# Performance work log

Measured on AMD Instinct MI355X. Metric: run time of the kernel, lower is better.

Reference implementation:

```python
import jax, jax.numpy as jnp
import numpy as np

N = 50000      # nodes
E = 800000     # edges (avg degree 16)
D = 64         # dim_inner
L = 2          # layers_mp
OUT = 2        # dim_out (fraud / not fraud)
LN_EPS = 1e-5


def setup_inputs() -> dict:
    key = jax.random.key(0)
    ks = jax.random.split(key, 12)
    rn = lambda k, shape: jax.random.normal(k, shape, dtype=jnp.float32) * 0.05
    return {
        "x": jax.random.normal(ks[0], (N, D), dtype=jnp.float32),
        "edge_attr": jax.random.normal(ks[1], (E, D), dtype=jnp.float32),
        "edge_index": jax.random.randint(ks[2], (2, E), 0, N),
        # GINEConv inner MLP: Linear(D,D) -> ReLU -> Linear(D,D), stacked over L layers
        "gine_w1": rn(ks[3], (L, D, D)), "gine_b1": jnp.zeros((L, D), jnp.float32),
        "gine_w2": rn(ks[4], (L, D, D)), "gine_b2": jnp.zeros((L, D), jnp.float32),
        # edge-update MLP: Linear(3D,D) -> ReLU -> Linear(D,D)
        "em_w1": rn(ks[5], (L, 3 * D, D)), "em_b1": jnp.zeros((L, D), jnp.float32),
        "em_w2": rn(ks[6], (L, D, D)), "em_b2": jnp.zeros((L, D), jnp.float32),
        # per-layer LayerNorm params
        "ln_g": jnp.ones((L, D), jnp.float32), "ln_b": jnp.zeros((L, D), jnp.float32),
        # post_mp head: Linear(D, OUT)
        "head_w": rn(ks[7], (D, OUT)), "head_b": jnp.zeros((OUT,), jnp.float32),
    }


def _layernorm(h, g, b):
    mu = h.mean(axis=-1, keepdims=True)
    var = h.var(axis=-1, keepdims=True)
    return (h - mu) * jax.lax.rsqrt(var + LN_EPS) * g + b


def reference(x, edge_attr, edge_index, gine_w1, gine_b1, gine_w2, gine_b2,
              em_w1, em_b1, em_w2, em_b2, ln_g, ln_b, head_w, head_b):
    src, dst = edge_index[0], edge_index[1]
    e = edge_attr
    for i in range(L):
        # GINEConv: sum_{j->i} relu(x_j + e_ji), eps=0 so (1+eps)*x_i = x_i
        msg = jax.nn.relu(x[src] + e)                         # [E, D] gather + fuse
        agg = jax.ops.segment_sum(msg, dst, num_segments=N)   # [N, D] scatter-add
        h = x + agg
        h = jax.nn.relu(h @ gine_w1[i] + gine_b1[i]) @ gine_w2[i] + gine_b2[i]
        # norm -> activation (dropout p=0 in eval)
        x = jax.nn.relu(_layernorm(h, ln_g[i], ln_b[i]))
        # edge update: e = e + emlp(cat[x_src, x_dst, e]) / 2
        cat = jnp.concatenate([x[src], x[dst], e], axis=-1)   # [E, 3D]
        e = e + (jax.nn.relu(cat @ em_w1[i] + em_b1[i]) @ em_w2[i] + em_b2[i]) * 0.5
    # post_mp head on node features
    return x @ head_w + head_b
```

## Files before the change

### kernel.cpp

```cpp
#include <hip/hip_runtime.h>
#include <hip/hip_bf16.h>

#define NN 50000
#define NE 800000
#define D 64
#define K3 (3 * D)
#define LNEPS 1e-5f
#define STR 68
#define SINB 200
#define SHB 72
#define SEB 68

typedef __attribute__((ext_vector_type(8))) short bf16x8;
typedef __attribute__((ext_vector_type(4))) float f32x4;

__device__ __forceinline__ unsigned cvt2(float lo, float hi) {
  __hip_bfloat162 h = __float22bfloat162_rn(make_float2(lo, hi));
  return *(unsigned*)&h;
}
__device__ __forceinline__ unsigned short f2bf(float f) {
  __hip_bfloat16 h = __float2bfloat16(f);
  return *(unsigned short*)&h;
}
__device__ __forceinline__ float bf2f(unsigned short s) {
  return __uint_as_float((unsigned)s << 16);
}

#define FMA4x4(v, w)                                                  \
  a0.x = fmaf(v.x, w.x, a0.x); a0.y = fmaf(v.x, w.y, a0.y);           \
  a0.z = fmaf(v.x, w.z, a0.z); a0.w = fmaf(v.x, w.w, a0.w);           \
  a1.x = fmaf(v.y, w.x, a1.x); a1.y = fmaf(v.y, w.y, a1.y);           \
  a1.z = fmaf(v.y, w.z, a1.z); a1.w = fmaf(v.y, w.w, a1.w);           \
  a2.x = fmaf(v.z, w.x, a2.x); a2.y = fmaf(v.z, w.y, a2.y);           \
  a2.z = fmaf(v.z, w.z, a2.z); a2.w = fmaf(v.z, w.w, a2.w);           \
  a3.x = fmaf(v.w, w.x, a3.x); a3.y = fmaf(v.w, w.y, a3.y);           \
  a3.z = fmaf(v.w, w.z, a3.z); a3.w = fmaf(v.w, w.w, a3.w);

#define FMA2x4(v, w)                                                  \
  a0.x = fmaf(v.x, w.x, a0.x); a0.y = fmaf(v.x, w.y, a0.y);           \
  a0.z = fmaf(v.x, w.z, a0.z); a0.w = fmaf(v.x, w.w, a0.w);           \
  a1.x = fmaf(v.y, w.x, a1.x); a1.y = fmaf(v.y, w.y, a1.y);           \
  a1.z = fmaf(v.y, w.z, a1.z); a1.w = fmaf(v.y, w.w, a1.w);

#define HSTORE_RELU(buf)                                              \
  buf[(j0+0)*STR + t0+0] = fmaxf(a0.x, 0.f);                          \
  buf[(j0+1)*STR + t0+0] = fmaxf(a0.y, 0.f);                          \
  buf[(j0+2)*STR + t0+0] = fmaxf(a0.z, 0.f);                          \
  buf[(j0+3)*STR + t0+0] = fmaxf(a0.w, 0.f);                          \
  buf[(j0+0)*STR + t0+1] = fmaxf(a1.x, 0.f);                          \
  buf[(j0+1)*STR + t0+1] = fmaxf(a1.y, 0.f);                          \
  buf[(j0+2)*STR + t0+1] = fmaxf(a1.z, 0.f);                          \
  buf[(j0+3)*STR + t0+1] = fmaxf(a1.w, 0.f);                          \
  buf[(j0+0)*STR + t0+2] = fmaxf(a2.x, 0.f);                          \
  buf[(j0+1)*STR + t0+2] = fmaxf(a2.y, 0.f);                          \
  buf[(j0+2)*STR + t0+2] = fmaxf(a2.z, 0.f);                          \
  buf[(j0+3)*STR + t0+2] = fmaxf(a2.w, 0.f);                          \
  buf[(j0+0)*STR + t0+3] = fmaxf(a3.x, 0.f);                          \
  buf[(j0+1)*STR + t0+3] = fmaxf(a3.y, 0.f);                          \
  buf[(j0+2)*STR + t0+3] = fmaxf(a3.z, 0.f);                          \
  buf[(j0+3)*STR + t0+3] = fmaxf(a3.w, 0.f);

__global__ __launch_bounds__(256) void count_kernel(
    const int* __restrict__ dst, int* __restrict__ deg) {
  int e = blockIdx.x * 256 + threadIdx.x;
  if (e < NE) atomicAdd(&deg[dst[e]], 1);
}

__global__ __launch_bounds__(1024) void scan_reduce_kernel(
    const int* __restrict__ deg, int* __restrict__ bsum) {
  __shared__ int sS[16];
  int i = blockIdx.x * 1024 + threadIdx.x;
  int v = (i < NN) ? deg[i] : 0;
#pragma unroll
  for (int o = 32; o > 0; o >>= 1) v += __shfl_down(v, o, 64);
  if ((threadIdx.x & 63) == 0) sS[threadIdx.x >> 6] = v;
  __syncthreads();
  if (threadIdx.x == 0) {
    int s = 0;
#pragma unroll
    for (int k = 0; k < 16; ++k) s += sS[k];
    bsum[blockIdx.x] = s;
  }
}

__global__ __launch_bounds__(1024) void scan_final_kernel(
    const int* __restrict__ deg, const int* __restrict__ bsum,
    int* __restrict__ off, int* __restrict__ cur) {
  __shared__ int sD[1024];
  __shared__ int sOfs;
  const int t = threadIdx.x;
  const int b = blockIdx.x;
  int i = b * 1024 + t;
  int v = (i < NN) ? deg[i] : 0;
  sD[t] = v;
  if (t == 0) {
    int o = 0;
    for (int k = 0; k < b; ++k) o += bsum[k];
    sOfs = o;
  }
  __syncthreads();
  for (int st = 1; st < 1024; st <<= 1) {
    int add = (t >= st) ? sD[t - st] : 0;
    __syncthreads();
    sD[t] += add;
    __syncthreads();
  }
  if (i < NN) {
    int excl = sOfs + sD[t] - v;
    off[i] = excl;
    cur[i] = excl;
    if (i == NN - 1) off[NN] = NE;
  }
}

__global__ __launch_bounds__(256) void fill_kernel(
    const int* __restrict__ src, const int* __restrict__ dst,
    int* __restrict__ cur, int2* __restrict__ epair,
    int* __restrict__ dcsr, int* __restrict__ pos) {
  int e = blockIdx.x * 256 + threadIdx.x;
  if (e < NE) {
    int d = dst[e];
    int p = atomicAdd(&cur[d], 1);
    epair[p] = make_int2(e, src[e]);
    dcsr[p] = d;
    pos[e] = p;
  }
}

__global__ __launch_bounds__(256) void permute_e_kernel(
    const float* __restrict__ e, const int* __restrict__ pos,
    unsigned short* __restrict__ ecsr) {
  int tid = blockIdx.x * 256 + threadIdx.x;
  int eid = tid >> 2, q = tid & 3;
  if (eid >= NE) return;
  int p = pos[eid];
  const float4* srcp = (const float4*)(e + (size_t)eid * D + q * 16);
  float4 v0 = srcp[0], v1 = srcp[1], v2 = srcp[2], v3 = srcp[3];
  uint4 u0, u1;
  u0.x = cvt2(v0.x, v0.y); u0.y = cvt2(v0.z, v0.w);
  u0.z = cvt2(v1.x, v1.y); u0.w = cvt2(v1.z, v1.w);
  u1.x = cvt2(v2.x, v2.y); u1.y = cvt2(v2.z, v2.w);
  u1.z = cvt2(v3.x, v3.y); u1.w = cvt2(v3.z, v3.w);
  uint4* dstp = (uint4*)(ecsr + (size_t)p * D + q * 16);
  dstp[0] = u0;
  dstp[1] = u1;
}

__global__ __launch_bounds__(256) void pack_weights_kernel(
    const float* __restrict__ w1, const float* __restrict__ w2,
    unsigned short* __restrict__ wB1, unsigned short* __restrict__ wB2) {
  int tid = blockIdx.x * 256 + threadIdx.x;
  const float* wsrc;
  unsigned short* wdst;
  int kb, j, slot;
  if (tid < 1536) {
    int nt = tid / 384, kk = (tid / 64) % 6, l = tid & 63;
    kb = kk * 32 + (l >> 4) * 8;
    j = nt * 16 + (l & 15);
    wsrc = w1; wdst = wB1; slot = tid;
  } else {
    int t = tid - 1536;
    int nt = t / 128, kk = (t / 64) & 1, l = t & 63;
    kb = kk * 32 + (l >> 4) * 8;
    j = nt * 16 + (l & 15);
    wsrc = w2; wdst = wB2; slot = t;
  }
  unsigned short b[8];
#pragma unroll
  for (int i = 0; i < 8; ++i) b[i] = f2bf(wsrc[(kb + i) * D + j]);
  uint4 v;
  v.x = (unsigned)b[0] | ((unsigned)b[1] << 16);
  v.y = (unsigned)b[2] | ((unsigned)b[3] << 16);
  v.z = (unsigned)b[4] | ((unsigned)b[5] << 16);
  v.w = (unsigned)b[6] | ((unsigned)b[7] << 16);
  *(uint4*)(wdst + (size_t)slot * 8) = v;
}

__device__ __forceinline__ void mlp_tail512(
    float* sIN, float* sH, float* sPS, float* sPQ, float* sMu, float* sRs,
    const float* __restrict__ w1, const float* __restrict__ b1,
    const float* __restrict__ w2, const float* __restrict__ b2,
    const float* __restrict__ g, const float* __restrict__ bln,
    float* __restrict__ xo, unsigned short* __restrict__ xob,
    const float* __restrict__ hw, const float* __restrict__ hb,
    float* __restrict__ outh,
    int n0, int tid) {
  __syncthreads();
  const int tj = tid & 15, tt = tid >> 4;
  const int j0 = tj * 4, t0 = tt * 2;
  float4 a0, a1;

  {
    float4 bv = *(const float4*)(b1 + j0);
    a0 = a1 = bv;
    for (int k = 0; k < D; ++k) {
      float4 w = *(const float4*)(w1 + k * D + j0);
      float2 v = *(const float2*)&sIN[k * STR + t0];
      FMA2x4(v, w)
    }
  }
  sH[(j0 + 0) * STR + t0 + 0] = fmaxf(a0.x, 0.f);
  sH[(j0 + 1) * STR + t0 + 0] = fmaxf(a0.y, 0.f);
  sH[(j0 + 2) * STR + t0 + 0] = fmaxf(a0.z, 0.f);
  sH[(j0 + 3) * STR + t0 + 0] = fmaxf(a0.w, 0.f);
  sH[(j0 + 0) * STR + t0 + 1] = fmaxf(a1.x, 0.f);
  sH[(j0 + 1) * STR + t0 + 1] = fmaxf(a1.y, 0.f);
  sH[(j0 + 2) * STR + t0 + 1] = fmaxf(a1.z, 0.f);
  sH[(j0 + 3) * STR + t0 + 1] = fmaxf(a1.w, 0.f);
  __syncthreads();

  {
    float4 bv = *(const float4*)(b2 + j0);
    a0 = a1 = bv;
    for (int k = 0; k < D; ++k) {
      float4 w = *(const float4*)(w2 + k * D + j0);
      float2 v = *(const float2*)&sH[k * STR + t0];
      FMA2x4(v, w)
    }
  }
  __syncthreads();
  *(float4*)&sH[(t0 + 0) * STR + j0] = a0;
  *(float4*)&sH[(t0 + 1) * STR + j0] = a1;
  __syncthreads();

  {
    const int t = tid & 63, p = tid >> 6;
    const float* r = &sH[t * STR + p * 8];
    float s = 0.f, q = 0.f;
#pragma unroll
    for (int i = 0; i < 8; ++i) { float v = r[i]; s += v; q = fmaf(v, v, q); }
    sPS[p * 64 + t] = s;
    sPQ[p * 64 + t] = q;
  }
  __syncthreads();
  if (tid < 64) {
    float s = 0.f, q = 0.f;
#pragma unroll
    for (int p = 0; p < 8; ++p) { s += sPS[p * 64 + tid]; q += sPQ[p * 64 + tid]; }
    float mu = s * (1.f / 64.f);
    float var = q * (1.f / 64.f) - mu * mu;
    sMu[tid] = mu;
    sRs[tid] = rsqrtf(var + LNEPS);
  }
  __syncthreads();

  {
    const int t = tid >> 3, c = (tid & 7) * 8;
    int node = n0 + t;
    if (node < NN) {
      float mu = sMu[t], rs = sRs[t];
      float4 v0 = *(const float4*)&sH[t * STR + c + 0];
      float4 v1 = *(const float4*)&sH[t * STR + c + 4];
      float4 g0v = *(const float4*)(g + c + 0);
      float4 g1v = *(const float4*)(g + c + 4);
      float4 b0v = *(const float4*)(bln + c + 0);
      float4 b1v = *(const float4*)(bln + c + 4);
      float4 r0, r1;
      r0.x = fmaxf(fmaf((v0.x - mu) * rs, g0v.x, b0v.x), 0.f);
      r0.y = fmaxf(fmaf((v0.y - mu) * rs, g0v.y, b0v.y), 0.f);
      r0.z = fmaxf(fmaf((v0.z - mu) * rs, g0v.z, b0v.z), 0.f);
      r0.w = fmaxf(fmaf((v0.w - mu) * rs, g0v.w, b0v.w), 0.f);
      r1.x = fmaxf(fmaf((v1.x - mu) * rs, g1v.x, b1v.x), 0.f);
      r1.y = fmaxf(fmaf((v1.y - mu) * rs, g1v.y, b1v.y), 0.f);
      r1.z = fmaxf(fmaf((v1.z - mu) * rs, g1v.z, b1v.z), 0.f);
      r1.w = fmaxf(fmaf((v1.w - mu) * rs, g1v.w, b1v.w), 0.f);
      if (outh) {
        float h0, h1;
        h0 = r0.x * hw[(c + 0) * 2 + 0] + r0.y * hw[(c + 1) * 2 + 0] +
             r0.z * hw[(c + 2) * 2 + 0] + r0.w * hw[(c + 3) * 2 + 0] +
             r1.x * hw[(c + 4) * 2 + 0] + r1.y * hw[(c + 5) * 2 + 0] +
             r1.z * hw[(c + 6) * 2 + 0] + r1.w * hw[(c + 7) * 2 + 0];
        h1 = r0.x * hw[(c + 0) * 2 + 1] + r0.y * hw[(c + 1) * 2 + 1] +
             r0.z * hw[(c + 2) * 2 + 1] + r0.w * hw[(c + 3) * 2 + 1] +
             r1.x * hw[(c + 4) * 2 + 1] + r1.y * hw[(c + 5) * 2 + 1] +
             r1.z * hw[(c + 6) * 2 + 1] + r1.w * hw[(c + 7) * 2 + 1];
#pragma unroll
        for (int o = 1; o < 8; o <<= 1) {
          h0 += __shfl_xor(h0, o, 64);
          h1 += __shfl_xor(h1, o, 64);
        }
        if ((tid & 7) == 0) {
          outh[node * 2 + 0] = h0 + hb[0];
          outh[node * 2 + 1] = h1 + hb[1];
        }
      } else {
        float* o = xo + (size_t)node * D + c;
        ((float4*)o)[0] = r0;
        ((float4*)o)[1] = r1;
        if (xob) {
          uint4 u;
          u.x = cvt2(r0.x, r0.y); u.y = cvt2(r0.z, r0.w);
          u.z = cvt2(r1.x, r1.y); u.w = cvt2(r1.z, r1.w);
          *(uint4*)(xob + (size_t)node * D + c) = u;
        }
      }
    }
  }
}

__global__ __launch_bounds__(512) void node_mlp_g0_kernel(
    const float* __restrict__ x, const unsigned short* __restrict__ ecsr,
    const int2* __restrict__ epair, const int* __restrict__ off,
    const float* __restrict__ w1, const float* __restrict__ b1,
    const float* __restrict__ w2, const float* __restrict__ b2,
    const float* __restrict__ g, const float* __restrict__ bln,
    float* __restrict__ xo, unsigned short* __restrict__ xob) {
  __shared__ float sIN[D * STR];
  __shared__ float sH[D * STR];
  __shared__ float sPS[512], sPQ[512], sMu[64], sRs[64];
  const int tid = threadIdx.x;
  const int n0 = blockIdx.x * 64;
  const int wv = tid >> 6, lane = tid & 63;
  for (int q = 0; q < 8; ++q) {
    int t = wv * 8 + q;
    int node = n0 + t;
    float acc = 0.f;
    if (node < NN) {
      acc = x[(size_t)node * D + lane];
      int beg = off[node], end = off[node + 1];
      const unsigned short* er = ecsr + (size_t)beg * D + lane;
      int cnt = end - beg, i = 0;
      for (; i + 3 < cnt; i += 4) {
        int s0 = epair[beg + i + 0].y, s1 = epair[beg + i + 1].y;
        int s2 = epair[beg + i + 2].y, s3 = epair[beg + i + 3].y;
        float xa = x[(size_t)s0 * D + lane], ea = bf2f(er[(size_t)(i + 0) * D]);
        float xb = x[(size_t)s1 * D + lane], eb = bf2f(er[(size_t)(i + 1) * D]);
        float xc = x[(size_t)s2 * D + lane], ec = bf2f(er[(size_t)(i + 2) * D]);
        float xd = x[(size_t)s3 * D + lane], ed = bf2f(er[(size_t)(i + 3) * D]);
        acc += (fmaxf(xa + ea, 0.f) + fmaxf(xb + eb, 0.f)) +
               (fmaxf(xc + ec, 0.f) + fmaxf(xd + ed, 0.f));
      }
      for (; i < cnt; ++i) {
        int s0 = epair[beg + i].y;
        acc += fmaxf(x[(size_t)s0 * D + lane] + bf2f(er[(size_t)i * D]), 0.f);
      }
    }
    sIN[lane * STR + t] = acc;
  }
  mlp_tail512(sIN, sH, sPS, sPQ, sMu, sRs, w1, b1, w2, b2, g, bln,
              xo, xob, nullptr, nullptr, nullptr, n0, tid);
}

__global__ __launch_bounds__(512) void node_mlp_g1_kernel(
    const float* __restrict__ x, const unsigned short* __restrict__ msg,
    const int* __restrict__ off,
    const float* __restrict__ w1, const float* __restrict__ b1,
    const float* __restrict__ w2, const float* __restrict__ b2,
    const float* __restrict__ g, const float* __restrict__ bln,
    const float* __restrict__ hw, const float* __restrict__ hb,
    float* __restrict__ outh) {
  __shared__ float sIN[D * STR];
  __shared__ float sH[D * STR];
  __shared__ float sPS[512], sPQ[512], sMu[64], sRs[64];
  const int tid = threadIdx.x;
  const int n0 = blockIdx.x * 64;
  const int wv = tid >> 6, lane = tid & 63;
  for (int q = 0; q < 8; ++q) {
    int t = wv * 8 + q;
    int node = n0 + t;
    float acc = 0.f;
    if (node < NN) {
      acc = x[(size_t)node * D + lane];
      int beg = off[node], end = off[node + 1];
      const unsigned short* mr = msg + (size_t)beg * D + lane;
      int cnt = end - beg, i = 0;
      for (; i + 3 < cnt; i += 4) {
        float m0 = bf2f(mr[(size_t)(i + 0) * D]);
        float m1 = bf2f(mr[(size_t)(i + 1) * D]);
        float m2 = bf2f(mr[(size_t)(i + 2) * D]);
        float m3 = bf2f(mr[(size_t)(i + 3) * D]);
        acc += (m0 + m1) + (m2 + m3);
      }
      for (; i < cnt; ++i) acc += bf2f(mr[(size_t)i * D]);
    }
    sIN[lane * STR + t] = acc;
  }
  mlp_tail512(sIN, sH, sPS, sPQ, sMu, sRs, w1, b1, w2, b2, g, bln,
              nullptr, nullptr, hw, hb, outh, n0, tid);
}

__global__ __launch_bounds__(256) void edge_mfma_csr_kernel(
    const unsigned short* __restrict__ x1b, const unsigned short* __restrict__ ecsr,
    const int2* __restrict__ epair, const int* __restrict__ dcsr,
    const unsigned short* __restrict__ wB1, const float* __restrict__ b1,
    const unsigned short* __restrict__ wB2, const float* __restrict__ b2,
    unsigned short* __restrict__ msg) {
  __shared__ unsigned short sIN[64 * SINB];
  __shared__ unsigned short sH[64 * SHB];

  const int tid = threadIdx.x;
  const int e0 = blockIdx.x * 64;
  const int lane = tid & 63;
  const int mt = tid >> 6;
  const int hl = lane >> 4;
  const int ll = lane & 15;

  {
    const int t = tid & 63, p = tid >> 6;
    int slot = e0 + t;
    int sN = epair[slot].y;
    int dN = dcsr[slot];
    const uint4* xs = (const uint4*)(x1b + (size_t)sN * D + p * 16);
    const uint4* xd = (const uint4*)(x1b + (size_t)dN * D + p * 16);
    const uint4* ec = (const uint4*)(ecsr + (size_t)slot * D + p * 16);
    uint4* r0 = (uint4*)(sIN + t * SINB + p * 16);
    uint4* r1 = (uint4*)(sIN + t * SINB + 64 + p * 16);
    uint4* r2 = (uint4*)(sIN + t * SINB + 128 + p * 16);
    uint4 a0v = xs[0], a1v = xs[1];
    uint4 b0v = xd[0], b1v = xd[1];
    uint4 c0v = ec[0], c1v = ec[1];
    r0[0] = a0v; r0[1] = a1v;
    r1[0] = b0v; r1[1] = b1v;
    r2[0] = c0v; r2[1] = c1v;
  }
  __syncthreads();

  f32x4 acc[4];
#pragma unroll
  for (int nt = 0; nt < 4; ++nt) {
    float b = b1[nt * 16 + ll];
    acc[nt].x = b; acc[nt].y = b; acc[nt].z = b; acc[nt].w = b;
  }
  {
    const unsigned short* aBase = sIN + (mt * 16 + ll) * SINB + hl * 8;
#pragma unroll
    for (int kk = 0; kk < 6; ++kk) {
      bf16x8 af = *(const bf16x8*)(aBase + kk * 32);
#pragma unroll
      for (int nt = 0; nt < 4; ++nt) {
        bf16x8 bf = *(const bf16x8*)(wB1 + ((size_t)(nt * 6 + kk) * 64 + lane) * 8);
        acc[nt] = __builtin_amdgcn_mfma_f32_16x16x32_bf16(af, bf, acc[nt], 0, 0, 0);
      }
    }
  }
#pragma unroll
  for (int nt = 0; nt < 4; ++nt)
#pragma unroll
    for (int r = 0; r < 4; ++r)
      sH[(mt * 16 + hl * 4 + r) * SHB + nt * 16 + ll] = f2bf(fmaxf(acc[nt][r], 0.f));
  __syncthreads();

  f32x4 acc2[4];
#pragma unroll
  for (int nt = 0; nt < 4; ++nt) {
    float b = b2[nt * 16 + ll];
    acc2[nt].x = b; acc2[nt].y = b; acc2[nt].z = b; acc2[nt].w = b;
  }
  {
    const unsigned short* hBase = sH + (mt * 16 + ll) * SHB + hl * 8;
#pragma unroll
    for (int kk = 0; kk < 2; ++kk) {
      bf16x8 af = *(const bf16x8*)(hBase + kk * 32);
#pragma unroll
      for (int nt = 0; nt < 4; ++nt) {
        bf16x8 bf = *(const bf16x8*)(wB2 + ((size_t)(nt * 2 + kk) * 64 + lane) * 8);
        acc2[nt] = __builtin_amdgcn_mfma_f32_16x16x32_bf16(af, bf, acc2[nt], 0, 0, 0);
      }
    }
  }

#pragma unroll
  for (int r = 0; r < 4; ++r) {
    int t = mt * 16 + hl * 4 + r;
    int slot = e0 + t;
    const unsigned short* xr = sIN + t * SINB;
    const unsigned short* er = sIN + t * SINB + 128;
    unsigned short* mr = msg + (size_t)slot * D;
#pragma unroll
    for (int nt = 0; nt < 4; ++nt) {
      int j = nt * 16 + ll;
      float xf = bf2f(xr[j]);
      float ef = bf2f(er[j]);
      mr[j] = f2bf(fmaxf(xf + fmaf(0.5f, acc2[nt][r], ef), 0.f));
    }
  }
}

__global__ __launch_bounds__(256) void scatter_kernel(
    const float* __restrict__ x, const float* __restrict__ e,
    const int* __restrict__ src, const int* __restrict__ dst,
    float* __restrict__ agg) {
  int tid = blockIdx.x * blockDim.x + threadIdx.x;
  if (tid >= NE * 16) return;
  int eid = tid >> 4, q = tid & 15;
  int s = src[eid], d = dst[eid];
  float4 xv = ((const float4*)(x + (size_t)s * D))[q];
  float4 ev = ((const float4*)(e + (size_t)eid * D))[q];
  float* a = agg + (size_t)d * D + q * 4;
  atomicAdd(a + 0, fmaxf(xv.x + ev.x, 0.f));
  atomicAdd(a + 1, fmaxf(xv.y + ev.y, 0.f));
  atomicAdd(a + 2, fmaxf(xv.z + ev.z, 0.f));
  atomicAdd(a + 3, fmaxf(xv.w + ev.w, 0.f));
}

__device__ __forceinline__ void mlp_tail256(
    float* sIN, float* sH, float* sPS, float* sPQ, float* sMu, float* sRs,
    const float* __restrict__ w1, const float* __restrict__ b1,
    const float* __restrict__ w2, const float* __restrict__ b2,
    const float* __restrict__ g, const float* __restrict__ bln,
    float* __restrict__ xo, int n0, int tid) {
  __syncthreads();
  const int tj = tid & 15, tt = tid >> 4;
  const int j0 = tj * 4, t0 = tt * 4;
  float4 a0, a1, a2, a3;
  {
    float4 bv = *(const float4*)(b1 + j0);
    a0 = a1 = a2 = a3 = bv;
    for (int k = 0; k < D; ++k) {
      float4 w = *(const float4*)(w1 + k * D + j0);
      float4 v = *(const float4*)&sIN[k * STR + t0];
      FMA4x4(v, w)
    }
  }
  HSTORE_RELU(sH)
  __syncthreads();
  {
    float4 bv = *(const float4*)(b2 + j0);
    a0 = a1 = a2 = a3 = bv;
    for (int k = 0; k < D; ++k) {
      float4 w = *(const float4*)(w2 + k * D + j0);
      float4 v = *(const float4*)&sH[k * STR + t0];
      FMA4x4(v, w)
    }
  }
  __syncthreads();
  *(float4*)&sH[(t0 + 0) * STR + j0] = a0;
  *(float4*)&sH[(t0 + 1) * STR + j0] = a1;
  *(float4*)&sH[(t0 + 2) * STR + j0] = a2;
  *(float4*)&sH[(t0 + 3) * STR + j0] = a3;
  __syncthreads();
  {
    const int t = tid & 63, p = tid >> 6;
    const float* r = &sH[t * STR + p * 16];
    float s = 0.f, q = 0.f;
#pragma unroll
    for (int i = 0; i < 16; ++i) { float v = r[i]; s += v; q = fmaf(v, v, q); }
    sPS[p * 64 + t] = s;
    sPQ[p * 64 + t] = q;
  }
  __syncthreads();
  if (tid < 64) {
    float s = sPS[tid] + sPS[64 + tid] + sPS[128 + tid] + sPS[192 + tid];
    float q = sPQ[tid] + sPQ[64 + tid] + sPQ[128 + tid] + sPQ[192 + tid];
    float mu = s * (1.f / 64.f);
    float var = q * (1.f / 64.f) - mu * mu;
    sMu[tid] = mu;
    sRs[tid] = rsqrtf(var + LNEPS);
  }
  __syncthreads();
  {
    const int t = tid >> 2, c = (tid & 3) * 16;
    int node = n0 + t;
    if (node < NN) {
      float mu = sMu[t], rs = sRs[t];
      float* o = xo + (size_t)node * D + c;
#pragma unroll
      for (int i = 0; i < 4; ++i) {
        float4 v = *(const float4*)&sH[t * STR + c + i * 4];
        float4 gv = *(const float4*)(g + c + i * 4);
        float4 bv = *(const float4*)(bln + c + i * 4);
        float4 r;
        r.x = fmaxf(fmaf((v.x - mu) * rs, gv.x, bv.x), 0.f);
        r.y = fmaxf(fmaf((v.y - mu) * rs, gv.y, bv.y), 0.f);
        r.z = fmaxf(fmaf((v.z - mu) * rs, gv.z, bv.z), 0.f);
        r.w = fmaxf(fmaf((v.w - mu) * rs, gv.w, bv.w), 0.f);
        ((float4*)o)[i] = r;
      }
    }
  }
}

__global__ __launch_bounds__(256) void node_mlp_kernel(
    const float* __restrict__ x, const float* __restrict__ agg,
    const float* __restrict__ w1, const float* __restrict__ b1,
    const float* __restrict__ w2, const float* __restrict__ b2,
    const float* __restrict__ g, const float* __restrict__ bln,
    float* __restrict__ xo) {
  __shared__ float sIN[D * STR];
  __shared__ float sH[D * STR];
  __shared__ float sPS[256], sPQ[256], sMu[64], sRs[64];
  const int tid = threadIdx.x;
  const int n0 = blockIdx.x * 64;
  {
    const int t = tid & 63, p = tid >> 6;
    int node = n0 + t;
    int cn = node < NN ? node : 0;
    const float* xr = x + (size_t)cn * D + p * 16;
    const float* ar = agg + (size_t)cn * D + p * 16;
#pragma unroll
    for (int i = 0; i < 4; ++i) {
      float4 xv = ((const float4*)xr)[i];
      float4 av = ((const float4*)ar)[i];
      int k = p * 16 + i * 4;
      sIN[(k + 0) * STR + t] = xv.x + av.x;
      sIN[(k + 1) * STR + t] = xv.y + av.y;
      sIN[(k + 2) * STR + t] = xv.z + av.z;
      sIN[(k + 3) * STR + t] = xv.w + av.w;
    }
  }
  mlp_tail256(sIN, sH, sPS, sPQ, sMu, sRs, w1, b1, w2, b2, g, bln, xo, n0, tid);
}

__global__ __launch_bounds__(256) void edge_mfma_atomic_kernel(
    const float* __restrict__ x, const float* __restrict__ e,
    const int* __restrict__ src, const int* __restrict__ dst,
    const unsigned short* __restrict__ wB1, const float* __restrict__ b1,
    const unsigned short* __restrict__ wB2, const float* __restrict__ b2,
    float* __restrict__ agg) {
  __shared__ unsigned short sIN[64 * SINB];
  __shared__ unsigned short sH[64 * SHB];
  __shared__ float sE[64 * SEB];
  const int tid = threadIdx.x;
  const int e0 = blockIdx.x * 64;
  const int lane = tid & 63;
  const int mt = tid >> 6;
  const int hl = lane >> 4;
  const int ll = lane & 15;
  {
    const int t = tid & 63, p = tid >> 6;
    int eid = e0 + t;
    int sN = src[eid], dN = dst[eid];
    const float* g0 = x + (size_t)sN * D + p * 16;
    const float* g1 = x + (size_t)dN * D + p * 16;
    const float* g2 = e + (size_t)eid * D + p * 16;
    unsigned short* row = sIN + t * SINB + p * 16;
#pragma unroll
    for (int i = 0; i < 4; ++i) {
      float4 v0 = ((const float4*)g0)[i];
      float4 v1 = ((const float4*)g1)[i];
      float4 v2 = ((const float4*)g2)[i];
      uint2 u;
      u.x = cvt2(v0.x, v0.y); u.y = cvt2(v0.z, v0.w);
      *(uint2*)(row + i * 4) = u;
      u.x = cvt2(v1.x, v1.y); u.y = cvt2(v1.z, v1.w);
      *(uint2*)(row + 64 + i * 4) = u;
      u.x = cvt2(v2.x, v2.y); u.y = cvt2(v2.z, v2.w);
      *(uint2*)(row + 128 + i * 4) = u;
      *(float4*)&sE[t * SEB + p * 16 + i * 4] = v2;
    }
  }
  __syncthreads();
  f32x4 acc[4];
#pragma unroll
  for (int nt = 0; nt < 4; ++nt) {
    float b = b1[nt * 16 + ll];
    acc[nt].x = b; acc[nt].y = b; acc[nt].z = b; acc[nt].w = b;
  }
  {
    const unsigned short* aBase = sIN + (mt * 16 + ll) * SINB + hl * 8;
#pragma unroll
    for (int kk = 0; kk < 6; ++kk) {
      bf16x8 af = *(const bf16x8*)(aBase + kk * 32);
#pragma unroll
      for (int nt = 0; nt < 4; ++nt) {
        bf16x8 bf = *(const bf16x8*)(wB1 + ((size_t)(nt * 6 + kk) * 64 + lane) * 8);
        acc[nt] = __builtin_amdgcn_mfma_f32_16x16x32_bf16(af, bf, acc[nt], 0, 0, 0);
      }
    }
  }
#pragma unroll
  for (int nt = 0; nt < 4; ++nt)
#pragma unroll
    for (int r = 0; r < 4; ++r)
      sH[(mt * 16 + hl * 4 + r) * SHB + nt * 16 + ll] = f2bf(fmaxf(acc[nt][r], 0.f));
  __syncthreads();
  f32x4 acc2[4];
#pragma unroll
  for (int nt = 0; nt < 4; ++nt) {
    float b = b2[nt * 16 + ll];
    acc2[nt].x = b; acc2[nt].y = b; acc2[nt].z = b; acc2[nt].w = b;
  }
  {
    const unsigned short* hBase = sH + (mt * 16 + ll) * SHB + hl * 8;
#pragma unroll
    for (int kk = 0; kk < 2; ++kk) {
      bf16x8 af = *(const bf16x8*)(hBase + kk * 32);
#pragma unroll
      for (int nt = 0; nt < 4; ++nt) {
        bf16x8 bf = *(const bf16x8*)(wB2 + ((size_t)(nt * 2 + kk) * 64 + lane) * 8);
        acc2[nt] = __builtin_amdgcn_mfma_f32_16x16x32_bf16(af, bf, acc2[nt], 0, 0, 0);
      }
    }
  }
#pragma unroll
  for (int r = 0; r < 4; ++r) {
    int t = mt * 16 + hl * 4 + r;
    int eid = e0 + t;
    int sN = src[eid], dN = dst[eid];
    const float* xr = x + (size_t)sN * D;
    const float* er = &sE[t * SEB];
    float* ar = agg + (size_t)dN * D;
#pragma unroll
    for (int nt = 0; nt < 4; ++nt) {
      int j = nt * 16 + ll;
      atomicAdd(ar + j, fmaxf(xr[j] + fmaf(0.5f, acc2[nt][r], er[j]), 0.f));
    }
  }
}

__global__ __launch_bounds__(256) void head_kernel(
    const float* __restrict__ x, const float* __restrict__ w,
    const float* __restrict__ b, float* __restrict__ out) {
  int nid = blockIdx.x * blockDim.x + threadIdx.x;
  if (nid >= NN) return;
  const float* xr = x + (size_t)nid * D;
  float a0 = b[0], a1 = b[1];
  for (int k = 0; k < D; ++k) {
    float v = xr[k];
    a0 = fmaf(v, w[k * 2 + 0], a0);
    a1 = fmaf(v, w[k * 2 + 1], a1);
  }
  out[nid * 2 + 0] = a0;
  out[nid * 2 + 1] = a1;
}

extern "C" void kernel_launch(void* const* d_in, const int* in_sizes, int n_in,
                              void* d_out, int out_size, void* d_ws, size_t ws_size,
                              hipStream_t stream) {
  const float* x0  = (const float*)d_in[0];
  const float* e0  = (const float*)d_in[1];
  const int*   ei  = (const int*)d_in[2];
  const float* gw1 = (const float*)d_in[3];
  const float* gb1 = (const float*)d_in[4];
  const float* gw2 = (const float*)d_in[5];
  const float* gb2 = (const float*)d_in[6];
  const float* ew1 = (const float*)d_in[7];
  const float* eb1 = (const float*)d_in[8];
  const float* ew2 = (const float*)d_in[9];
  const float* eb2 = (const float*)d_in[10];
  const float* lng = (const float*)d_in[11];
  const float* lnb = (const float*)d_in[12];
  const float* hw  = (const float*)d_in[13];
  const float* hb  = (const float*)d_in[14];
  float* out = (float*)d_out;

  char* ws = (char*)d_ws;
  const size_t SZ_X     = (size_t)NN * D * 4;
  const size_t OFF_X1   = 0;
  const size_t OFF_WB1  = OFF_X1 + SZ_X;
  const size_t OFF_WB2  = OFF_WB1 + 24576;
  const size_t OFF_DEG  = OFF_WB2 + 8192;
  const size_t OFF_OFFS = OFF_DEG + 200704;
  const size_t OFF_CUR  = OFF_OFFS + 200704;
  const size_t OFF_BSUM = OFF_CUR + 200704;
  const size_t OFF_EPAIR= OFF_BSUM + 512;
  const size_t OFF_DCSR = OFF_EPAIR + (size_t)NE * 8;
  const size_t OFF_POS  = OFF_DCSR + (size_t)NE * 4;
  const size_t OFF_X1B  = OFF_POS + (size_t)NE * 4;
  const size_t OFF_ECSR = OFF_X1B + (size_t)NN * D * 2;
  const size_t OFF_MSG  = OFF_ECSR + (size_t)NE * D * 2;
  const size_t NEED_A   = OFF_MSG + (size_t)NE * D * 2;

  float* x1   = (float*)(ws + OFF_X1);
  unsigned short* wB1 = (unsigned short*)(ws + OFF_WB1);
  unsigned short* wB2 = (unsigned short*)(ws + OFF_WB2);
  int* deg  = (int*)(ws + OFF_DEG);
  int* offs = (int*)(ws + OFF_OFFS);
  int* cur  = (int*)(ws + OFF_CUR);
  int* bsum = (int*)(ws + OFF_BSUM);
  int2* epair = (int2*)(ws + OFF_EPAIR);
  int* dcsr = (int*)(ws + OFF_DCSR);
  int* pos  = (int*)(ws + OFF_POS);
  unsigned short* x1b  = (unsigned short*)(ws + OFF_X1B);
  unsigned short* ecsr = (unsigned short*)(ws + OFF_ECSR);
  unsigned short* msg  = (unsigned short*)(ws + OFF_MSG);

  const int* src = ei;
  const int* dst = ei + NE;

  const int nodeBlocks = (NN + 63) / 64;
  const int edgeBlocks = NE / 64;
  const int scanBlocks = (NN + 1023) / 1024;

  pack_weights_kernel<<<8, 256, 0, stream>>>(ew1, ew2, wB1, wB2);

  if (ws_size >= NEED_A) {
    hipMemsetAsync(deg, 0, (size_t)NN * 4, stream);
    count_kernel<<<(NE + 255) / 256, 256, 0, stream>>>(dst, deg);
    scan_reduce_kernel<<<scanBlocks, 1024, 0, stream>>>(deg, bsum);
    scan_final_kernel<<<scanBlocks, 1024, 0, stream>>>(deg, bsum, offs, cur);
    fill_kernel<<<(NE + 255) / 256, 256, 0, stream>>>(src, dst, cur, epair, dcsr, pos);

    permute_e_kernel<<<(NE * 4 + 255) / 256, 256, 0, stream>>>(e0, pos, ecsr);

    node_mlp_g0_kernel<<<nodeBlocks, 512, 0, stream>>>(
        x0, ecsr, epair, offs, gw1, gb1, gw2, gb2, lng, lnb, x1, x1b);

    edge_mfma_csr_kernel<<<edgeBlocks, 256, 0, stream>>>(
        x1b, ecsr, epair, dcsr, wB1, eb1, wB2, eb2, msg);

    node_mlp_g1_kernel<<<nodeBlocks, 512, 0, stream>>>(
        x1, msg, offs, gw1 + D * D, gb1 + D, gw2 + D * D, gb2 + D,
        lng + D, lnb + D, hw, hb, out);
  } else {
    float* agg = (float*)(ws + OFF_EPAIR);
    float* x2  = (float*)(ws + OFF_EPAIR + SZ_X);
    hipMemsetAsync(agg, 0, SZ_X, stream);
    scatter_kernel<<<(NE * 16 + 255) / 256, 256, 0, stream>>>(x0, e0, src, dst, agg);
    node_mlp_kernel<<<nodeBlocks, 256, 0, stream>>>(
        x0, agg, gw1, gb1, gw2, gb2, lng, lnb, x1);
    hipMemsetAsync(agg, 0, SZ_X, stream);
    edge_mfma_atomic_kernel<<<edgeBlocks, 256, 0, stream>>>(
        x1, e0, src, dst, wB1, eb1, wB2, eb2, agg);
    node_mlp_kernel<<<nodeBlocks, 256, 0, stream>>>(
        x1, agg, gw1 + D * D, gb1 + D, gw2 + D * D, gb2 + D, lng + D, lnb + D, x2);
    head_kernel<<<(NN + 255) / 256, 256, 0, stream>>>(x2, hw, hb, out);
  }
}
```

Measured before the change: 393.2 us.

## Fuse layer-1 message aggregation into edge kernel via segmented atomic reduction

The edge MLP kernel no longer writes per-edge bf16 messages for a later CSR gather. Because edges are already sorted by destination, it now reduces each block's 64 messages by destination segment in shared memory and atomically adds the partial sums into a float node aggregate. The second node kernel then reads just x+agg per node. This removes the 800k×64 message write and re-read, at the cost of zeroing a node-sized buffer, float atomics at block boundaries, a serial 64-step segment loop run by one wave, and extra syncs. hipMemsetAsync calls are also replaced by small zeroing kernels.

```diff
diff --git a/kernel.cpp b/kernel.cpp
--- a/kernel.cpp
+++ b/kernel.cpp
@@ -59,6 +59,15 @@
   buf[(j0+1)*STR + t0+3] = fmaxf(a3.y, 0.f);                          \
   buf[(j0+2)*STR + t0+3] = fmaxf(a3.z, 0.f);                          \
   buf[(j0+3)*STR + t0+3] = fmaxf(a3.w, 0.f);
+
+__global__ __launch_bounds__(256) void zero_int_kernel(int* __restrict__ p, int n) {
+  int i = blockIdx.x * 256 + threadIdx.x;
+  if (i < n) p[i] = 0;
+}
+__global__ __launch_bounds__(256) void zero_f4_kernel(float4* __restrict__ p, int n) {
+  int i = blockIdx.x * 256 + threadIdx.x;
+  if (i < n) p[i] = make_float4(0.f, 0.f, 0.f, 0.f);
+}
 
 __global__ __launch_bounds__(256) void count_kernel(
     const int* __restrict__ dst, int* __restrict__ deg) {
@@ -341,9 +350,8 @@
               xo, xob, nullptr, nullptr, nullptr, n0, tid);
 }
 
-__global__ __launch_bounds__(512) void node_mlp_g1_kernel(
-    const float* __restrict__ x, const unsigned short* __restrict__ msg,
-    const int* __restrict__ off,
+__global__ __launch_bounds__(512) void node_mlp1_kernel(
+    const float* __restrict__ x, const float* __restrict__ agg,
     const float* __restrict__ w1, const float* __restrict__ b1,
     const float* __restrict__ w2, const float* __restrict__ b2,
     const float* __restrict__ g, const float* __restrict__ bln,
@@ -354,39 +362,36 @@
   __shared__ float sPS[512], sPQ[512], sMu[64], sRs[64];
   const int tid = threadIdx.x;
   const int n0 = blockIdx.x * 64;
-  const int wv = tid >> 6, lane = tid & 63;
-  for (int q = 0; q < 8; ++q) {
-    int t = wv * 8 + q;
+  {
+    const int t = tid & 63, p = tid >> 6;
     int node = n0 + t;
-    float acc = 0.f;
-    if (node < NN) {
-      acc = x[(size_t)node * D + lane];
-      int beg = off[node], end = off[node + 1];
-      const unsigned short* mr = msg + (size_t)beg * D + lane;
-      int cnt = end - beg, i = 0;
-      for (; i + 3 < cnt; i += 4) {
-        float m0 = bf2f(mr[(size_t)(i + 0) * D]);
-        float m1 = bf2f(mr[(size_t)(i + 1) * D]);
-        float m2 = bf2f(mr[(size_t)(i + 2) * D]);
-        float m3 = bf2f(mr[(size_t)(i + 3) * D]);
-        acc += (m0 + m1) + (m2 + m3);
-      }
-      for (; i < cnt; ++i) acc += bf2f(mr[(size_t)i * D]);
-    }
-    sIN[lane * STR + t] = acc;
+    int cn = node < NN ? node : 0;
+    const float* xr = x + (size_t)cn * D + p * 8;
+    const float* ar = agg + (size_t)cn * D + p * 8;
+#pragma unroll
+    for (int i = 0; i < 2; ++i) {
+      float4 xv = ((const float4*)xr)[i];
+      float4 av = ((const float4*)ar)[i];
+      int k = p * 8 + i * 4;
+      sIN[(k + 0) * STR + t] = xv.x + av.x;
+      sIN[(k + 1) * STR + t] = xv.y + av.y;
+      sIN[(k + 2) * STR + t] = xv.z + av.z;
+      sIN[(k + 3) * STR + t] = xv.w + av.w;
+    }
   }
   mlp_tail512(sIN, sH, sPS, sPQ, sMu, sRs, w1, b1, w2, b2, g, bln,
               nullptr, nullptr, hw, hb, outh, n0, tid);
 }
 
-__global__ __launch_bounds__(256) void edge_mfma_csr_kernel(
+__global__ __launch_bounds__(256) void edge_mfma_seg_kernel(
     const unsigned short* __restrict__ x1b, const unsigned short* __restrict__ ecsr,
     const int2* __restrict__ epair, const int* __restrict__ dcsr,
     const unsigned short* __restrict__ wB1, const float* __restrict__ b1,
     const unsigned short* __restrict__ wB2, const float* __restrict__ b2,
-    unsigned short* __restrict__ msg) {
+    float* __restrict__ agg) {
   __shared__ unsigned short sIN[64 * SINB];
   __shared__ unsigned short sH[64 * SHB];
+  __shared__ int sDst[64];
 
   const int tid = threadIdx.x;
   const int e0 = blockIdx.x * 64;
@@ -400,6 +405,7 @@
     int slot = e0 + t;
     int sN = epair[slot].y;
     int dN = dcsr[slot];
+    if (p == 0) sDst[t] = dN;
     const uint4* xs = (const uint4*)(x1b + (size_t)sN * D + p * 16);
     const uint4* xd = (const uint4*)(x1b + (size_t)dN * D + p * 16);
     const uint4* ec = (const uint4*)(ecsr + (size_t)slot * D + p * 16);
@@ -459,20 +465,58 @@
     }
   }
 
-#pragma unroll
-  for (int r = 0; r < 4; ++r) {
-    int t = mt * 16 + hl * 4 + r;
-    int slot = e0 + t;
-    const unsigned short* xr = sIN + t * SINB;
-    const unsigned short* er = sIN + t * SINB + 128;
-    unsigned short* mr = msg + (size_t)slot * D;
-#pragma unroll
-    for (int nt = 0; nt < 4; ++nt) {
-      int j = nt * 16 + ll;
-      float xf = bf2f(xr[j]);
-      float ef = bf2f(er[j]);
-      mr[j] = f2bf(fmaxf(xf + fmaf(0.5f, acc2[nt][r], ef), 0.f));
-    }
+  float m0x, m0y, m0z, m0w, m1x, m1y, m1z, m1w;
+  float m2x, m2y, m2z, m2w, m3x, m3y, m3z, m3w;
+  {
+    const unsigned short* x0r = sIN + (mt * 16 + hl * 4 + 0) * SINB;
+    const unsigned short* x1r = sIN + (mt * 16 + hl * 4 + 1) * SINB;
+    const unsigned short* x2r = sIN + (mt * 16 + hl * 4 + 2) * SINB;
+    const unsigned short* x3r = sIN + (mt * 16 + hl * 4 + 3) * SINB;
+#define MSG(xr, nt, r) fmaxf(bf2f(xr[nt * 16 + ll]) + fmaf(0.5f, acc2[nt][r], bf2f(xr[128 + nt * 16 + ll])), 0.f)
+    m0x = MSG(x0r, 0, 0); m0y = MSG(x0r, 1, 0); m0z = MSG(x0r, 2, 0); m0w = MSG(x0r, 3, 0);
+    m1x = MSG(x1r, 0, 1); m1y = MSG(x1r, 1, 1); m1z = MSG(x1r, 2, 1); m1w = MSG(x1r, 3, 1);
+    m2x = MSG(x2r, 0, 2); m2y = MSG(x2r, 1, 2); m2z = MSG(x2r, 2, 2); m2w = MSG(x2r, 3, 2);
+    m3x = MSG(x3r, 0, 3); m3y = MSG(x3r, 1, 3); m3z = MSG(x3r, 2, 3); m3w = MSG(x3r, 3, 3);
+#undef MSG
+  }
+  __syncthreads();
+
+  float* msgF = (float*)sIN;
+  {
+    int tb = mt * 16 + hl * 4;
+    msgF[(tb + 0) * 65 + 0 * 16 + ll] = m0x;
+    msgF[(tb + 0) * 65 + 1 * 16 + ll] = m0y;
+    msgF[(tb + 0) * 65 + 2 * 16 + ll] = m0z;
+    msgF[(tb + 0) * 65 + 3 * 16 + ll] = m0w;
+    msgF[(tb + 1) * 65 + 0 * 16 + ll] = m1x;
+    msgF[(tb + 1) * 65 + 1 * 16 + ll] = m1y;
+    msgF[(tb + 1) * 65 + 2 * 16 + ll] = m1z;
+    msgF[(tb + 1) * 65 + 3 * 16 + ll] = m1w;
+    msgF[(tb + 2) * 65 + 0 * 16 + ll] = m2x;
+    msgF[(tb + 2) * 65 + 1 * 16 + ll] = m2y;
+    msgF[(tb + 2) * 65 + 2 * 16 + ll] = m2z;
+    msgF[(tb + 2) * 65 + 3 * 16 + ll] = m2w;
+    msgF[(tb + 3) * 65 + 0 * 16 + ll] = m3x;
+    msgF[(tb + 3) * 65 + 1 * 16 + ll] = m3y;
+    msgF[(tb + 3) * 65 + 2 * 16 + ll] = m3z;
+    msgF[(tb + 3) * 65 + 3 * 16 + ll] = m3w;
+  }
+  __syncthreads();
+
+  if (tid < 64) {
+    int j = tid;
+    int cur = sDst[0];
+    float sum = msgF[j];
+    for (int t = 1; t < 64; ++t) {
+      int d = sDst[t];
+      if (d != cur) {
+        atomicAdd(&agg[(size_t)cur * D + j], sum);
+        cur = d;
+        sum = 0.f;
+      }
+      sum += msgF[t * 65 + j];
+    }
+    atomicAdd(&agg[(size_t)cur * D + j], sum);
   }
 }
 
@@ -747,9 +791,9 @@
   const size_t OFF_DCSR = OFF_EPAIR + (size_t)NE * 8;
   const size_t OFF_POS  = OFF_DCSR + (size_t)NE * 4;
   const size_t OFF_X1B  = OFF_POS + (size_t)NE * 4;
-  const size_t OFF_ECSR = OFF_X1B + (size_t)NN * D * 2;
-  const size_t OFF_MSG  = OFF_ECSR + (size_t)NE * D * 2;
-  const size_t NEED_A   = OFF_MSG + (size_t)NE * D * 2;
+  const size_t OFF_AGG  = OFF_X1B + (size_t)NN * D * 2;
+  const size_t OFF_ECSR = OFF_AGG + SZ_X;
+  const size_t NEED_A   = OFF_ECSR + (size_t)NE * D * 2;
 
   float* x1   = (float*)(ws + OFF_X1);
   unsigned short* wB1 = (unsigned short*)(ws + OFF_WB1);
@@ -762,8 +806,8 @@
   int* dcsr = (int*)(ws + OFF_DCSR);
   int* pos  = (int*)(ws + OFF_POS);
   unsigned short* x1b  = (unsigned short*)(ws + OFF_X1B);
+  float* agg = (float*)(ws + OFF_AGG);
   unsigned short* ecsr = (unsigned short*)(ws + OFF_ECSR);
-  unsigned short* msg  = (unsigned short*)(ws + OFF_MSG);
 
   const int* src = ei;
   const int* dst = ei + NE;
@@ -775,7 +819,7 @@
   pack_weights_kernel<<<8, 256, 0, stream>>>(ew1, ew2, wB1, wB2);
 
   if (ws_size >= NEED_A) {
-    hipMemsetAsync(deg, 0, (size_t)NN * 4, stream);
+    zero_int_kernel<<<(NN + 255) / 256, 256, 0, stream>>>(deg, NN);
     count_kernel<<<(NE + 255) / 256, 256, 0, stream>>>(dst, deg);
     scan_reduce_kernel<<<scanBlocks, 1024, 0, stream>>>(deg, bsum);
     scan_final_kernel<<<scanBlocks, 1024, 0, stream>>>(deg, bsum, offs, cur);
@@ -783,27 +827,32 @@
 
     permute_e_kernel<<<(NE * 4 + 255) / 256, 256, 0, stream>>>(e0, pos, ecsr);
 
+    zero_f4_kernel<<<(NN * D / 4 + 255) / 256, 256, 0, stream>>>(
+        (float4*)agg, NN * D / 4);
+
     node_mlp_g0_kernel<<<nodeBlocks, 512, 0, stream>>>(
         x0, ecsr, epair, offs, gw1, gb1, gw2, gb2, lng, lnb, x1, x1b);
 
-    edge_mfma_csr_kernel<<<edgeBlocks, 256, 0, stream>>>(
-        x1b, ecsr, epair, dcsr, wB1, eb1, wB2, eb2, msg);
-
-    node_mlp_g1_kernel<<<nodeBlocks, 512, 0, stream>>>(
-        x1, msg, offs, gw1 + D * D, gb1 + D, gw2 + D * D, gb2 + D,
+    edge_mfma_seg_kernel<<<edgeBlocks, 256, 0, stream>>>(
+        x1b, ecsr, epair, dcsr, wB1, eb1, wB2, eb2, agg);
+
+    node_mlp1_kernel<<<nodeBlocks, 512, 0, stream>>>(
+        x1, agg, gw1 + D * D, gb1 + D, gw2 + D * D, gb2 + D,
         lng + D, lnb + D, hw, hb, out);
   } else {
-    float* agg = (float*)(ws + OFF_EPAIR);
-    float* x2  = (float*)(ws + OFF_EPAIR + SZ_X);
-    hipMemsetAsync(agg, 0, SZ_X, stream);
-    scatter_kernel<<<(NE * 16 + 255) / 256, 256, 0, stream>>>(x0, e0, src, dst, agg);
+    float* fagg = (float*)(ws + OFF_EPAIR);
+    float* x2   = (float*)(ws + OFF_EPAIR + SZ_X);
+    zero_f4_kernel<<<(NN * D / 4 + 255) / 256, 256, 0, stream>>>(
+        (float4*)fagg, NN * D / 4);
+    scatter_kernel<<<(NE * 16 + 255) / 256, 256, 0, stream>>>(x0, e0, src, dst, fagg);
     node_mlp_kernel<<<nodeBlocks, 256, 0, stream>>>(
-        x0, agg, gw1, gb1, gw2, gb2, lng, lnb, x1);
-    hipMemsetAsync(agg, 0, SZ_X, stream);
+        x0, fagg, gw1, gb1, gw2, gb2, lng, lnb, x1);
+    zero_f4_kernel<<<(NN * D / 4 + 255) / 256, 256, 0, stream>>>(
+        (float4*)fagg, NN * D / 4);
     edge_mfma_atomic_kernel<<<edgeBlocks, 256, 0, stream>>>(
-        x1, e0, src, dst, wB1, eb1, wB2, eb2, agg);
+        x1, e0, src, dst, wB1, eb1, wB2, eb2, fagg);
     node_mlp_kernel<<<nodeBlocks, 256, 0, stream>>>(
-        x1, agg, gw1 + D * D, gb1 + D, gw2 + D * D, gb2 + D, lng + D, lnb + D, x2);
+        x1, fagg, gw1 + D * D, gb1 + D, gw2 + D * D, gb2 + D, lng + D, lnb + D, x2);
     head_kernel<<<(NN + 255) / 256, 256, 0, stream>>>(x2, hw, hb, out);
   }
 }
```

Measured after the change: 423.8 us. 7.8% more time.
